# Performance work log

Measured on AMD Instinct MI355X. Metric: run time of the kernel, lower is better.

## Reference

```python
import jax, jax.numpy as jnp
import numpy as np

B, T, D = 2, 2048, 1024
H = 16
DH = D // H


def setup_inputs() -> dict:
    key = jax.random.key(0)
    ks = jax.random.split(key, 6)
    s = 1.0 / np.sqrt(D)
    return {
        "input_emb": jax.random.normal(ks[0], (B, T, D), dtype=jnp.float32),
        "W_key": jax.random.normal(ks[1], (D, D), dtype=jnp.float32) * s,
        "W_query": jax.random.normal(ks[2], (D, D), dtype=jnp.float32) * s,
        "W_value": jax.random.normal(ks[3], (D, D), dtype=jnp.float32) * s,
        "W_out": jax.random.normal(ks[4], (D, D), dtype=jnp.float32) * s,
        "b_out": jnp.zeros((D,), dtype=jnp.float32),
    }


def reference(input_emb, W_key, W_query, W_value, W_out, b_out):
    b, t, _ = input_emb.shape
    # projections (no bias on K/Q/V, matching bias_on=False)
    k = (input_emb @ W_key).reshape(b, t, H, DH).transpose(0, 2, 1, 3)    # [b,h,t,dh]
    q = (input_emb @ W_query).reshape(b, t, H, DH).transpose(0, 2, 1, 3)
    v = (input_emb @ W_value).reshape(b, t, H, DH).transpose(0, 2, 1, 3)
    # NOTE: source computes K @ Q^T (not Q @ K^T) — reproduce faithfully.
    scores = jnp.einsum("bhid,bhjd->bhij", k, q) / jnp.sqrt(jnp.float32(DH))
    mask = jnp.triu(jnp.ones((t, t), dtype=bool), k=1)                    # True where j > i
    scores = jnp.where(mask, -jnp.inf, scores)
    attn = jax.nn.softmax(scores, axis=-1)                                # softmax over j (query axis)
    ctx = jnp.einsum("bhij,bhjd->bhid", attn, v)                          # [b,h,t,dh]
    ctx = ctx.transpose(0, 2, 1, 3).reshape(b, t, H * DH)                 # [b,t,d]
    return ctx @ W_out + b_out
```

## Files before the change

kernel.cpp:

```cpp
#include <hip/hip_runtime.h>
#include <cstdint>
#include <cstddef>

#define T_SEQ 2048
#define DMODEL 1024
#define NHEAD 16
#define DHEAD 64
#define BATCH 2
#define MROWS (BATCH * T_SEQ)

typedef __attribute__((ext_vector_type(8))) short bf16x8;
typedef __attribute__((ext_vector_type(4))) float f32x4;
typedef unsigned int u32;

__device__ __forceinline__ unsigned short f2bf(float f) {
  u32 u = __float_as_uint(f);
  u32 r = (u + 0x7FFFu + ((u >> 16) & 1u)) >> 16;
  return (unsigned short)r;
}

__device__ __forceinline__ u32 cvtpk(float a, float b) {
  u32 r;
  asm("v_cvt_pk_bf16_f32 %0, %1, %2" : "=v"(r) : "v"(a), "v"(b));
  return r;
}

__device__ __forceinline__ void gl_lds16(const unsigned short* g, unsigned short* l) {
  __builtin_amdgcn_global_load_lds(
      (const __attribute__((address_space(1))) u32*)g,
      (__attribute__((address_space(3))) u32*)l, 16, 0, 0);
}

__global__ void k_cvt(const float* __restrict__ src, unsigned short* __restrict__ dst, int n) {
  int i = (blockIdx.x * 256 + threadIdx.x) * 4;
  if (i + 3 < n) {
    float4 v = *reinterpret_cast<const float4*>(src + i);
    ushort4 o;
    o.x = f2bf(v.x); o.y = f2bf(v.y); o.z = f2bf(v.z); o.w = f2bf(v.w);
    *reinterpret_cast<ushort4*>(dst + i) = o;
  }
}

__global__ void k_tc4(const float* __restrict__ W0, const float* __restrict__ W1,
                      const float* __restrict__ W2, const float* __restrict__ W3,
                      unsigned short* __restrict__ T0, unsigned short* __restrict__ T1,
                      unsigned short* __restrict__ T2, unsigned short* __restrict__ T3) {
  const int z = blockIdx.z;
  const float* W = (z == 0) ? W0 : (z == 1) ? W1 : (z == 2) ? W2 : W3;
  unsigned short* Wt = (z == 0) ? T0 : (z == 1) ? T1 : (z == 2) ? T2 : T3;
  __shared__ float tile[32][33];
  const int c0 = blockIdx.x * 32, r0 = blockIdx.y * 32;
  const int tx = threadIdx.x & 31, ty = threadIdx.x >> 5;
#pragma unroll
  for (int i = ty; i < 32; i += 8)
    tile[i][tx] = W[(size_t)(r0 + i) * DMODEL + c0 + tx];
  __syncthreads();
#pragma unroll
  for (int i = ty; i < 32; i += 8)
    Wt[(size_t)(c0 + i) * DMODEL + r0 + tx] = f2bf(tile[tx][i]);
}

__global__ __launch_bounds__(256, 2)
void k_gemm_qkv(const unsigned short* __restrict__ Xb,
                const unsigned short* __restrict__ Wkt,
                const unsigned short* __restrict__ Wqt,
                const unsigned short* __restrict__ Wvt,
                unsigned short* __restrict__ Qr,
                unsigned short* __restrict__ Kr,
                unsigned short* __restrict__ Vt)
{
  __shared__ __align__(16) unsigned short As[128 * 32];
  __shared__ __align__(16) unsigned short Bs[128 * 32];
  const int z = blockIdx.z;
  const unsigned short* Bt = (z == 0) ? Wkt : (z == 1) ? Wqt : Wvt;

  const int tid = threadIdx.x;
  const int lane = tid & 63, w = tid >> 6;
  const int wr = w >> 1, wc = w & 1;
  const int l15 = lane & 15, l4 = lane >> 4;
  const int m0 = blockIdx.y * 128, n0 = blockIdx.x * 128;

  f32x4 acc[4][4] = {};

  for (int k0 = 0; k0 < DMODEL; k0 += 32) {
#pragma unroll
    for (int i = 0; i < 2; ++i) {
      int c = i * 256 + tid;
      int row = c >> 2, cc = c & 3;
      gl_lds16(Xb + (size_t)(m0 + row) * DMODEL + k0 + cc * 8, As + c * 8);
      gl_lds16(Bt + (size_t)(n0 + row) * DMODEL + k0 + cc * 8, Bs + c * 8);
    }
    __syncthreads();
    bf16x8 af[4], bfr[4];
#pragma unroll
    for (int mi = 0; mi < 4; ++mi)
      af[mi] = *reinterpret_cast<const bf16x8*>(As + (wr * 64 + mi * 16 + l15) * 32 + l4 * 8);
#pragma unroll
    for (int ni = 0; ni < 4; ++ni)
      bfr[ni] = *reinterpret_cast<const bf16x8*>(Bs + (wc * 64 + ni * 16 + l15) * 32 + l4 * 8);
#pragma unroll
    for (int mi = 0; mi < 4; ++mi)
#pragma unroll
      for (int ni = 0; ni < 4; ++ni)
        acc[mi][ni] = __builtin_amdgcn_mfma_f32_16x16x32_bf16(af[mi], bfr[ni], acc[mi][ni], 0, 0, 0);
    __syncthreads();
  }

  if (z < 2) {
    unsigned short* C = (z == 0) ? Qr : Kr;
#pragma unroll
    for (int mi = 0; mi < 4; ++mi)
#pragma unroll
      for (int ni = 0; ni < 4; ++ni) {
        const int col = n0 + wc * 64 + ni * 16 + l15;
        const int rowb = m0 + wr * 64 + mi * 16 + l4 * 4;
#pragma unroll
        for (int r = 0; r < 4; ++r)
          C[(size_t)(rowb + r) * DMODEL + col] = f2bf(acc[mi][ni][r]);
      }
  } else {
#pragma unroll
    for (int mi = 0; mi < 4; ++mi)
#pragma unroll
      for (int ni = 0; ni < 4; ++ni) {
        const int col = n0 + wc * 64 + ni * 16 + l15;
        const int h = col >> 6, dh = col & 63;
        const int rowb = m0 + wr * 64 + mi * 16 + l4 * 4;
        const int b = rowb >> 11, t = rowb & (T_SEQ - 1);
        const int tl = t & 63;
        const int tp = (t & ~63) | (tl & 32) | ((tl & 12) << 1) | ((tl & 16) >> 2);
        unsigned short* p = Vt + ((size_t)(b * NHEAD + h) * DHEAD + dh) * T_SEQ + tp;
        ushort4 pkv;
        pkv.x = f2bf(acc[mi][ni][0]); pkv.y = f2bf(acc[mi][ni][1]);
        pkv.z = f2bf(acc[mi][ni][2]); pkv.w = f2bf(acc[mi][ni][3]);
        *reinterpret_cast<ushort4*>(p) = pkv;
      }
  }
}

__global__ __launch_bounds__(512, 2)
void k_attn(const unsigned short* __restrict__ Qr,
            const unsigned short* __restrict__ Kr,
            const unsigned short* __restrict__ Vp,
            unsigned short* __restrict__ ctx)
{
  __shared__ __align__(16) char lds[65536];
  const int tid = threadIdx.x;
  const int lane = tid & 63, w = tid >> 6;
  const int l15 = lane & 15, l4 = lane >> 4;

  const int x = blockIdx.x;
  const int xcd = x & 7, idx = x >> 3;
  const int bh = xcd + 8 * (idx & 3);
  const int cpair = idx >> 2;
  const int b = bh >> 4, h = bh & 15;

  const unsigned short* Qbase = Qr + (size_t)b * T_SEQ * DMODEL + h * DHEAD;
  const unsigned short* Kbase = Kr + (size_t)b * T_SEQ * DMODEL + h * DHEAD;
  const unsigned short* Vbase = Vp + (size_t)bh * DHEAD * T_SEQ;
  unsigned short* obase = ctx + (size_t)b * T_SEQ * DMODEL + h * DHEAD;

  const float SC = 0.18033688011112042f;
  const float M0 = 12.0f;
  const int srow = tid >> 3, scb = tid & 7;
  const int scolE = (scb ^ (srow & 7)) << 3;

  const int sw = (l15 & 7) << 4;
  const char* aK0 = lds + l15 * 128 + ((l4 * 16) ^ sw);
  const char* aK1 = lds + l15 * 128 + (((64 + l4 * 16)) ^ sw);

  const unsigned short* kp = Kbase + (size_t)srow * DMODEL + scolE;
  const unsigned short* vpb = Vbase + (size_t)srow * T_SEQ + scolE;

#define KRD(P, st, ni, v1) (*reinterpret_cast<const bf16x8*>(((v1) ? aK1 : aK0) + (P) * 16384 + (st) * 8192 + (ni) * 2048))
#define VRD(P, st, df, hk) (*reinterpret_cast<const bf16x8*>(((hk) ? aK1 : aK0) + 32768 + (P) * 16384 + (st) * 8192 + (df) * 2048))

#define GROUP_BODY(g, P)                                                          \
    {                                                                             \
      const int kv0 = (g) * 128;                                                  \
      const bool diag = ((g) == NG - 1);                                          \
      __builtin_amdgcn_sched_barrier(0);                                          \
      asm volatile("s_waitcnt vmcnt(0)" ::: "memory");                            \
      __builtin_amdgcn_sched_barrier(0);                                          \
      __builtin_amdgcn_s_barrier();                                               \
      __builtin_amdgcn_sched_barrier(0);                                          \
      if ((g) + 1 < NG) {                                                         \
        unsigned short* Kn = (unsigned short*)(lds + ((P) ^ 1) * 16384);          \
        unsigned short* Vn = (unsigned short*)(lds + 32768 + ((P) ^ 1) * 16384);  \
        gl_lds16(kstage, Kn + tid * 8);                                           \
        gl_lds16(kstage + 64 * DMODEL, Kn + 4096 + tid * 8);                      \
        gl_lds16(vstage, Vn + tid * 8);                                           \
        gl_lds16(vstage + 64, Vn + 4096 + tid * 8);                               \
        kstage += 128 * DMODEL; vstage += 128;                                    \
      }                                                                           \
      __builtin_amdgcn_sched_barrier(0);                                          \
      const bool a1 = !diag || (w >= 4);                                          \
      const int nlim0 = (diag && w < 4) ? (w + 1) : 4;                            \
      const int nlim1 = (diag && w >= 4) ? (w - 3) : 4;                           \
      f32x4 S[2][4] = {};                                                         \
      __builtin_amdgcn_s_setprio(1);                                              \
      _Pragma("unroll")                                                           \
      for (int ni = 0; ni < 4; ++ni)                                              \
        if (ni < nlim0) {                                                         \
          S[0][ni] = __builtin_amdgcn_mfma_f32_16x16x32_bf16(KRD(P, 0, ni, 0), qf[0], S[0][ni], 0, 0, 0); \
          S[0][ni] = __builtin_amdgcn_mfma_f32_16x16x32_bf16(KRD(P, 0, ni, 1), qf[1], S[0][ni], 0, 0, 0); \
        }                                                                         \
      if (a1) {                                                                   \
        _Pragma("unroll")                                                         \
        for (int ni = 0; ni < 4; ++ni)                                            \
          if (ni < nlim1) {                                                       \
            S[1][ni] = __builtin_amdgcn_mfma_f32_16x16x32_bf16(KRD(P, 1, ni, 0), qf[0], S[1][ni], 0, 0, 0); \
            S[1][ni] = __builtin_amdgcn_mfma_f32_16x16x32_bf16(KRD(P, 1, ni, 1), qf[1], S[1][ni], 0, 0, 0); \
          }                                                                       \
      }                                                                           \
      __builtin_amdgcn_s_setprio(0);                                              \
      if (diag) {                                                                 \
        const int st = (w < 4) ? 0 : 1;                                           \
        const int kvst = kv0 + st * 64;                                           \
        const int nl = (w < 4) ? nlim0 : nlim1;                                   \
        _Pragma("unroll")                                                         \
        for (int ni = 0; ni < 4; ++ni)                                            \
          if (ni < nl) {                                                          \
            _Pragma("unroll")                                                     \
            for (int r = 0; r < 4; ++r)                                           \
              if (kvst + ni * 16 + l4 * 4 + r > qrow) S[st][ni][r] = -INFINITY;   \
          }                                                                       \
      }                                                                           \
      union __align__(16) PW { u32 u[2][2][4]; bf16x8 v[2][2]; } pw = {};         \
      _Pragma("unroll")                                                           \
      for (int ni = 0; ni < 4; ++ni)                                              \
        if (ni < nlim0) {                                                         \
          const float p0 = __builtin_amdgcn_exp2f(__builtin_fmaf(S[0][ni][0], SC, -M0)); \
          const float p1 = __builtin_amdgcn_exp2f(__builtin_fmaf(S[0][ni][1], SC, -M0)); \
          const float p2 = __builtin_amdgcn_exp2f(__builtin_fmaf(S[0][ni][2], SC, -M0)); \
          const float p3 = __builtin_amdgcn_exp2f(__builtin_fmaf(S[0][ni][3], SC, -M0)); \
          lP += (p0 + p1) + (p2 + p3);                                            \
          pw.u[0][ni >> 1][(ni & 1) * 2]     = cvtpk(p0, p1);                     \
          pw.u[0][ni >> 1][(ni & 1) * 2 + 1] = cvtpk(p2, p3);                     \
        }                                                                         \
      if (a1) {                                                                   \
        _Pragma("unroll")                                                         \
        for (int ni = 0; ni < 4; ++ni)                                            \
          if (ni < nlim1) {                                                       \
            const float p0 = __builtin_amdgcn_exp2f(__builtin_fmaf(S[1][ni][0], SC, -M0)); \
            const float p1 = __builtin_amdgcn_exp2f(__builtin_fmaf(S[1][ni][1], SC, -M0)); \
            const float p2 = __builtin_amdgcn_exp2f(__builtin_fmaf(S[1][ni][2], SC, -M0)); \
            const float p3 = __builtin_amdgcn_exp2f(__builtin_fmaf(S[1][ni][3], SC, -M0)); \
            lP += (p0 + p1) + (p2 + p3);                                          \
            pw.u[1][ni >> 1][(ni & 1) * 2]     = cvtpk(p0, p1);                   \
            pw.u[1][ni >> 1][(ni & 1) * 2 + 1] = cvtpk(p2, p3);                   \
          }                                                                       \
      }                                                                           \
      __builtin_amdgcn_s_setprio(1);                                              \
      {                                                                           \
        const int hkl0 = (diag && w < 4) ? ((nlim0 + 1) >> 1) : 2;                \
        _Pragma("unroll")                                                         \
        for (int hk = 0; hk < 2; ++hk)                                            \
          if (hk < hkl0) {                                                        \
            _Pragma("unroll")                                                     \
            for (int df = 0; df < 4; ++df)                                        \
              O[df] = __builtin_amdgcn_mfma_f32_16x16x32_bf16(VRD(P, 0, df, hk), pw.v[0][hk], O[df], 0, 0, 0); \
          }                                                                       \
      }                                                                           \
      if (a1) {                                                                   \
        const int hkl1 = (diag && w >= 4) ? ((nlim1 + 1) >> 1) : 2;               \
        _Pragma("unroll")                                                         \
        for (int hk = 0; hk < 2; ++hk)                                            \
          if (hk < hkl1) {                                                        \
            _Pragma("unroll")                                                     \
            for (int df = 0; df < 4; ++df)                                        \
              O[df] = __builtin_amdgcn_mfma_f32_16x16x32_bf16(VRD(P, 1, df, hk), pw.v[1][hk], O[df], 0, 0, 0); \
          }                                                                       \
      }                                                                           \
      __builtin_amdgcn_s_setprio(0);                                              \
      __builtin_amdgcn_sched_barrier(0);                                          \
    }

  for (int half = 0; half < 2; ++half) {
    const int c = half ? (15 - cpair) : cpair;
    const int q0w = c * 128 + w * 16;
    const int NG = c + 1;
    const int qrow = q0w + l15;

    bf16x8 qf[2];
#pragma unroll
    for (int ks = 0; ks < 2; ++ks)
      qf[ks] = *reinterpret_cast<const bf16x8*>(
          Qbase + (size_t)(q0w + l15) * DMODEL + ks * 32 + l4 * 8);

    __builtin_amdgcn_sched_barrier(0);
    __builtin_amdgcn_s_barrier();
    __builtin_amdgcn_sched_barrier(0);
    {
      unsigned short* Ks = (unsigned short*)(lds);
      unsigned short* Vs = (unsigned short*)(lds + 32768);
      gl_lds16(kp, Ks + tid * 8);
      gl_lds16(kp + 64 * DMODEL, Ks + 4096 + tid * 8);
      gl_lds16(vpb, Vs + tid * 8);
      gl_lds16(vpb + 64, Vs + 4096 + tid * 8);
    }
    const unsigned short* kstage = kp + 128 * DMODEL;
    const unsigned short* vstage = vpb + 128;

    f32x4 O[4] = {};
    float lP = 0.f;

    for (int g2 = 0; g2 < NG; g2 += 2) {
      GROUP_BODY(g2, 0)
      if (g2 + 1 < NG) GROUP_BODY(g2 + 1, 1)
    }

    float lS = lP;
    lS += __shfl_xor(lS, 16);
    lS += __shfl_xor(lS, 32);
    const float rinv = 1.0f / lS;
#pragma unroll
    for (int df = 0; df < 4; ++df) {
      ushort4 o;
      o.x = f2bf(O[df][0] * rinv);
      o.y = f2bf(O[df][1] * rinv);
      o.z = f2bf(O[df][2] * rinv);
      o.w = f2bf(O[df][3] * rinv);
      *reinterpret_cast<ushort4*>(obase + (size_t)qrow * DMODEL + df * 16 + l4 * 4) = o;
    }
  }
#undef GROUP_BODY
#undef KRD
#undef VRD
}

__global__ __launch_bounds__(256, 2)
void k_gemm_out(const unsigned short* __restrict__ Ab,
                const unsigned short* __restrict__ Bt,
                const float* __restrict__ bias,
                float* __restrict__ C)
{
  __shared__ __align__(16) unsigned short As[128 * 32];
  __shared__ __align__(16) unsigned short Bs[128 * 32];
  const int tid = threadIdx.x;
  const int lane = tid & 63, w = tid >> 6;
  const int wr = w >> 1, wc = w & 1;
  const int l15 = lane & 15, l4 = lane >> 4;
  const int m0 = blockIdx.y * 128, n0 = blockIdx.x * 128;

  f32x4 acc[4][4] = {};

  for (int k0 = 0; k0 < DMODEL; k0 += 32) {
#pragma unroll
    for (int i = 0; i < 2; ++i) {
      int c = i * 256 + tid;
      int row = c >> 2, cc = c & 3;
      gl_lds16(Ab + (size_t)(m0 + row) * DMODEL + k0 + cc * 8, As + c * 8);
      gl_lds16(Bt + (size_t)(n0 + row) * DMODEL + k0 + cc * 8, Bs + c * 8);
    }
    __syncthreads();
    bf16x8 af[4], bfr[4];
#pragma unroll
    for (int mi = 0; mi < 4; ++mi)
      af[mi] = *reinterpret_cast<const bf16x8*>(As + (wr * 64 + mi * 16 + l15) * 32 + l4 * 8);
#pragma unroll
    for (int ni = 0; ni < 4; ++ni)
      bfr[ni] = *reinterpret_cast<const bf16x8*>(Bs + (wc * 64 + ni * 16 + l15) * 32 + l4 * 8);
#pragma unroll
    for (int mi = 0; mi < 4; ++mi)
#pragma unroll
      for (int ni = 0; ni < 4; ++ni)
        acc[mi][ni] = __builtin_amdgcn_mfma_f32_16x16x32_bf16(af[mi], bfr[ni], acc[mi][ni], 0, 0, 0);
    __syncthreads();
  }

#pragma unroll
  for (int mi = 0; mi < 4; ++mi)
#pragma unroll
    for (int ni = 0; ni < 4; ++ni) {
      const int col = n0 + wc * 64 + ni * 16 + l15;
      const float bv = bias[col];
      const int rowb = m0 + wr * 64 + mi * 16 + l4 * 4;
#pragma unroll
      for (int r = 0; r < 4; ++r)
        C[(size_t)(rowb + r) * DMODEL + col] = acc[mi][ni][r] + bv;
    }
}

extern "C" void kernel_launch(void* const* d_in, const int* in_sizes, int n_in,
                              void* d_out, int out_size, void* d_ws, size_t ws_size,
                              hipStream_t stream) {
  const float* X  = (const float*)d_in[0];
  const float* Wk = (const float*)d_in[1];
  const float* Wq = (const float*)d_in[2];
  const float* Wv = (const float*)d_in[3];
  const float* Wo = (const float*)d_in[4];
  const float* bo = (const float*)d_in[5];
  float* out = (float*)d_out;

  char* ws = (char*)d_ws;
  const size_t MB = 1024 * 1024;
  unsigned short* Xb  = (unsigned short*)(ws + 0 * MB);
  unsigned short* Wkt = (unsigned short*)(ws + 8 * MB);
  unsigned short* Wqt = (unsigned short*)(ws + 10 * MB);
  unsigned short* Wvt = (unsigned short*)(ws + 12 * MB);
  unsigned short* Wot = (unsigned short*)(ws + 14 * MB);
  unsigned short* Qr  = (unsigned short*)(ws + 16 * MB);
  unsigned short* Kr  = (unsigned short*)(ws + 24 * MB);
  unsigned short* Vt  = (unsigned short*)(ws + 32 * MB);
  unsigned short* Ctx = (unsigned short*)(ws + 40 * MB);

  k_cvt<<<4096, 256, 0, stream>>>(X, Xb, MROWS * DMODEL);
  k_tc4<<<dim3(32, 32, 4), 256, 0, stream>>>(Wk, Wq, Wv, Wo, Wkt, Wqt, Wvt, Wot);

  k_gemm_qkv<<<dim3(8, 32, 3), 256, 0, stream>>>(Xb, Wkt, Wqt, Wvt, Qr, Kr, Vt);
  k_attn<<<dim3(256), 512, 0, stream>>>(Qr, Kr, Vt, Ctx);
  k_gemm_out<<<dim3(8, 32), 256, 0, stream>>>(Ctx, Wot, bo, out);
}
```

Measured before the change: 107.3 us.

## Split attention waves over KV halves with two query tiles and LDS reduction

```diff
diff --git a/kernel.cpp b/kernel.cpp
--- a/kernel.cpp
+++ b/kernel.cpp
@@ -148,6 +148,7 @@
   const int tid = threadIdx.x;
   const int lane = tid & 63, w = tid >> 6;
   const int l15 = lane & 15, l4 = lane >> 4;
+  const int wsub = w & 3, par = w >> 2;
 
   const int x = blockIdx.x;
   const int xcd = x & 7, idx = x >> 3;
@@ -166,14 +167,15 @@
   const int scolE = (scb ^ (srow & 7)) << 3;
 
   const int sw = (l15 & 7) << 4;
-  const char* aK0 = lds + l15 * 128 + ((l4 * 16) ^ sw);
-  const char* aK1 = lds + l15 * 128 + (((64 + l4 * 16)) ^ sw);
+  const char* base0 = lds + par * 8192 + l15 * 128 + ((l4 * 16) ^ sw);
+  const char* base1 = lds + par * 8192 + l15 * 128 + ((64 + l4 * 16) ^ sw);
 
   const unsigned short* kp = Kbase + (size_t)srow * DMODEL + scolE;
   const unsigned short* vpb = Vbase + (size_t)srow * T_SEQ + scolE;
 
-#define KRD(P, st, ni, v1) (*reinterpret_cast<const bf16x8*>(((v1) ? aK1 : aK0) + (P) * 16384 + (st) * 8192 + (ni) * 2048))
-#define VRD(P, st, df, hk) (*reinterpret_cast<const bf16x8*>(((hk) ? aK1 : aK0) + 32768 + (P) * 16384 + (st) * 8192 + (df) * 2048))
+#define MFMA16(a, bq, c) __builtin_amdgcn_mfma_f32_16x16x32_bf16((a), (bq), (c), 0, 0, 0)
+#define KRD(P, ni, v1) (*reinterpret_cast<const bf16x8*>(((v1) ? base1 : base0) + (P) * 16384 + (ni) * 2048))
+#define VRD(P, df, hk) (*reinterpret_cast<const bf16x8*>(((hk) ? base1 : base0) + 32768 + (P) * 16384 + (df) * 2048))
 
 #define GROUP_BODY(g, P)                                                          \
     {                                                                             \
@@ -194,99 +196,97 @@
         kstage += 128 * DMODEL; vstage += 128;                                    \
       }                                                                           \
       __builtin_amdgcn_sched_barrier(0);                                          \
-      const bool a1 = !diag || (w >= 4);                                          \
-      const int nlim0 = (diag && w < 4) ? (w + 1) : 4;                            \
-      const int nlim1 = (diag && w >= 4) ? (w - 3) : 4;                           \
-      f32x4 S[2][4] = {};                                                         \
+      int nl0 = 4, nl1 = 4;                                                       \
+      if (diag) {                                                                 \
+        nl0 = ((wsub * 32 + 15 - par * 64) >> 4) + 1;                             \
+        nl1 = ((wsub * 32 + 31 - par * 64) >> 4) + 1;                             \
+        nl0 = nl0 < 0 ? 0 : (nl0 > 4 ? 4 : nl0);                                  \
+        nl1 = nl1 < 0 ? 0 : (nl1 > 4 ? 4 : nl1);                                  \
+      }                                                                           \
+      f32x4 S0[4] = {}, S1[4] = {};                                               \
       __builtin_amdgcn_s_setprio(1);                                              \
       _Pragma("unroll")                                                           \
       for (int ni = 0; ni < 4; ++ni)                                              \
-        if (ni < nlim0) {                                                         \
-          S[0][ni] = __builtin_amdgcn_mfma_f32_16x16x32_bf16(KRD(P, 0, ni, 0), qf[0], S[0][ni], 0, 0, 0); \
-          S[0][ni] = __builtin_amdgcn_mfma_f32_16x16x32_bf16(KRD(P, 0, ni, 1), qf[1], S[0][ni], 0, 0, 0); \
+        if (ni < nl1) {                                                           \
+          const bf16x8 ka = KRD(P, ni, 0);                                        \
+          const bf16x8 kb = KRD(P, ni, 1);                                        \
+          if (ni < nl0) {                                                         \
+            S0[ni] = MFMA16(ka, qf[0][0], S0[ni]);                                \
+            S0[ni] = MFMA16(kb, qf[0][1], S0[ni]);                                \
+          }                                                                       \
+          S1[ni] = MFMA16(ka, qf[1][0], S1[ni]);                                  \
+          S1[ni] = MFMA16(kb, qf[1][1], S1[ni]);                                  \
         }                                                                         \
-      if (a1) {                                                                   \
-        _Pragma("unroll")                                                         \
-        for (int ni = 0; ni < 4; ++ni)                                            \
-          if (ni < nlim1) {                                                       \
-            S[1][ni] = __builtin_amdgcn_mfma_f32_16x16x32_bf16(KRD(P, 1, ni, 0), qf[0], S[1][ni], 0, 0, 0); \
-            S[1][ni] = __builtin_amdgcn_mfma_f32_16x16x32_bf16(KRD(P, 1, ni, 1), qf[1], S[1][ni], 0, 0, 0); \
-          }                                                                       \
-      }                                                                           \
       __builtin_amdgcn_s_setprio(0);                                              \
       if (diag) {                                                                 \
-        const int st = (w < 4) ? 0 : 1;                                           \
-        const int kvst = kv0 + st * 64;                                           \
-        const int nl = (w < 4) ? nlim0 : nlim1;                                   \
+        const int kvb = kv0 + par * 64;                                           \
         _Pragma("unroll")                                                         \
-        for (int ni = 0; ni < 4; ++ni)                                            \
-          if (ni < nl) {                                                          \
-            _Pragma("unroll")                                                     \
-            for (int r = 0; r < 4; ++r)                                           \
-              if (kvst + ni * 16 + l4 * 4 + r > qrow) S[st][ni][r] = -INFINITY;   \
+        for (int ni = 0; ni < 4; ++ni) {                                          \
+          _Pragma("unroll")                                                       \
+          for (int r = 0; r < 4; ++r) {                                           \
+            const int kvi = kvb + ni * 16 + l4 * 4 + r;                           \
+            if (ni < nl0 && kvi > qrow0) S0[ni][r] = -INFINITY;                   \
+            if (ni < nl1 && kvi > qrow1) S1[ni][r] = -INFINITY;                   \
           }                                                                       \
+        }                                                                         \
       }                                                                           \
-      union __align__(16) PW { u32 u[2][2][4]; bf16x8 v[2][2]; } pw = {};         \
+      PW pw0 = {}, pw1 = {};                                                      \
       _Pragma("unroll")                                                           \
-      for (int ni = 0; ni < 4; ++ni)                                              \
-        if (ni < nlim0) {                                                         \
-          const float p0 = __builtin_amdgcn_exp2f(__builtin_fmaf(S[0][ni][0], SC, -M0)); \
-          const float p1 = __builtin_amdgcn_exp2f(__builtin_fmaf(S[0][ni][1], SC, -M0)); \
-          const float p2 = __builtin_amdgcn_exp2f(__builtin_fmaf(S[0][ni][2], SC, -M0)); \
-          const float p3 = __builtin_amdgcn_exp2f(__builtin_fmaf(S[0][ni][3], SC, -M0)); \
-          lP += (p0 + p1) + (p2 + p3);                                            \
-          pw.u[0][ni >> 1][(ni & 1) * 2]     = cvtpk(p0, p1);                     \
-          pw.u[0][ni >> 1][(ni & 1) * 2 + 1] = cvtpk(p2, p3);                     \
+      for (int ni = 0; ni < 4; ++ni) {                                            \
+        if (ni < nl0) {                                                           \
+          const float p0 = __builtin_amdgcn_exp2f(__builtin_fmaf(S0[ni][0], SC, -M0)); \
+          const float p1 = __builtin_amdgcn_exp2f(__builtin_fmaf(S0[ni][1], SC, -M0)); \
+          const float p2 = __builtin_amdgcn_exp2f(__builtin_fmaf(S0[ni][2], SC, -M0)); \
+          const float p3 = __builtin_amdgcn_exp2f(__builtin_fmaf(S0[ni][3], SC, -M0)); \
+          lP0 += (p0 + p1) + (p2 + p3);                                           \
+          pw0.u[ni >> 1][(ni & 1) * 2]     = cvtpk(p0, p1);                       \
+          pw0.u[ni >> 1][(ni & 1) * 2 + 1] = cvtpk(p2, p3);                       \
         }                                                                         \
-      if (a1) {                                                                   \
-        _Pragma("unroll")                                                         \
-        for (int ni = 0; ni < 4; ++ni)                                            \
-          if (ni < nlim1) {                                                       \
-            const float p0 = __builtin_amdgcn_exp2f(__builtin_fmaf(S[1][ni][0], SC, -M0)); \
-            const float p1 = __builtin_amdgcn_exp2f(__builtin_fmaf(S[1][ni][1], SC, -M0)); \
-            const float p2 = __builtin_amdgcn_exp2f(__builtin_fmaf(S[1][ni][2], SC, -M0)); \
-            const float p3 = __builtin_amdgcn_exp2f(__builtin_fmaf(S[1][ni][3], SC, -M0)); \
-            lP += (p0 + p1) + (p2 + p3);                                          \
-            pw.u[1][ni >> 1][(ni & 1) * 2]     = cvtpk(p0, p1);                   \
-            pw.u[1][ni >> 1][(ni & 1) * 2 + 1] = cvtpk(p2, p3);                   \
-          }                                                                       \
+        if (ni < nl1) {                                                           \
+          const float p0 = __builtin_amdgcn_exp2f(__builtin_fmaf(S1[ni][0], SC, -M0)); \
+          const float p1 = __builtin_amdgcn_exp2f(__builtin_fmaf(S1[ni][1], SC, -M0)); \
+          const float p2 = __builtin_amdgcn_exp2f(__builtin_fmaf(S1[ni][2], SC, -M0)); \
+          const float p3 = __builtin_amdgcn_exp2f(__builtin_fmaf(S1[ni][3], SC, -M0)); \
+          lP1 += (p0 + p1) + (p2 + p3);                                           \
+          pw1.u[ni >> 1][(ni & 1) * 2]     = cvtpk(p0, p1);                       \
+          pw1.u[ni >> 1][(ni & 1) * 2 + 1] = cvtpk(p2, p3);                       \
+        }                                                                         \
       }                                                                           \
       __builtin_amdgcn_s_setprio(1);                                              \
       {                                                                           \
-        const int hkl0 = (diag && w < 4) ? ((nlim0 + 1) >> 1) : 2;                \
-        _Pragma("unroll")                                                         \
-        for (int hk = 0; hk < 2; ++hk)                                            \
-          if (hk < hkl0) {                                                        \
-            _Pragma("unroll")                                                     \
-            for (int df = 0; df < 4; ++df)                                        \
-              O[df] = __builtin_amdgcn_mfma_f32_16x16x32_bf16(VRD(P, 0, df, hk), pw.v[0][hk], O[df], 0, 0, 0); \
-          }                                                                       \
-      }                                                                           \
-      if (a1) {                                                                   \
-        const int hkl1 = (diag && w >= 4) ? ((nlim1 + 1) >> 1) : 2;               \
+        const int hkl0 = diag ? ((nl0 + 1) >> 1) : 2;                             \
+        const int hkl1 = diag ? ((nl1 + 1) >> 1) : 2;                             \
         _Pragma("unroll")                                                         \
         for (int hk = 0; hk < 2; ++hk)                                            \
           if (hk < hkl1) {                                                        \
             _Pragma("unroll")                                                     \
-            for (int df = 0; df < 4; ++df)                                        \
-              O[df] = __builtin_amdgcn_mfma_f32_16x16x32_bf16(VRD(P, 1, df, hk), pw.v[1][hk], O[df], 0, 0, 0); \
+            for (int df = 0; df < 4; ++df) {                                      \
+              const bf16x8 vv = VRD(P, df, hk);                                   \
+              if (hk < hkl0) O0[df] = MFMA16(vv, pw0.v[hk], O0[df]);              \
+              O1[df] = MFMA16(vv, pw1.v[hk], O1[df]);                             \
+            }                                                                     \
           }                                                                       \
       }                                                                           \
       __builtin_amdgcn_s_setprio(0);                                              \
       __builtin_amdgcn_sched_barrier(0);                                          \
     }
 
+  union __align__(16) PW { u32 u[2][4]; bf16x8 v[2]; };
+
   for (int half = 0; half < 2; ++half) {
     const int c = half ? (15 - cpair) : cpair;
-    const int q0w = c * 128 + w * 16;
+    const int q0w = c * 128 + wsub * 32;
     const int NG = c + 1;
-    const int qrow = q0w + l15;
-
-    bf16x8 qf[2];
-#pragma unroll
-    for (int ks = 0; ks < 2; ++ks)
-      qf[ks] = *reinterpret_cast<const bf16x8*>(
-          Qbase + (size_t)(q0w + l15) * DMODEL + ks * 32 + l4 * 8);
+    const int qrow0 = q0w + l15;
+    const int qrow1 = q0w + 16 + l15;
+
+    bf16x8 qf[2][2];
+#pragma unroll
+    for (int qm = 0; qm < 2; ++qm)
+#pragma unroll
+      for (int ks = 0; ks < 2; ++ks)
+        qf[qm][ks] = *reinterpret_cast<const bf16x8*>(
+            Qbase + (size_t)(q0w + qm * 16 + l15) * DMODEL + ks * 32 + l4 * 8);
 
     __builtin_amdgcn_sched_barrier(0);
     __builtin_amdgcn_s_barrier();
@@ -302,31 +302,63 @@
     const unsigned short* kstage = kp + 128 * DMODEL;
     const unsigned short* vstage = vpb + 128;
 
-    f32x4 O[4] = {};
-    float lP = 0.f;
+    f32x4 O0[4] = {}, O1[4] = {};
+    float lP0 = 0.f, lP1 = 0.f;
 
     for (int g2 = 0; g2 < NG; g2 += 2) {
       GROUP_BODY(g2, 0)
       if (g2 + 1 < NG) GROUP_BODY(g2 + 1, 1)
     }
 
-    float lS = lP;
-    lS += __shfl_xor(lS, 16);
-    lS += __shfl_xor(lS, 32);
-    const float rinv = 1.0f / lS;
-#pragma unroll
-    for (int df = 0; df < 4; ++df) {
-      ushort4 o;
-      o.x = f2bf(O[df][0] * rinv);
-      o.y = f2bf(O[df][1] * rinv);
-      o.z = f2bf(O[df][2] * rinv);
-      o.w = f2bf(O[df][3] * rinv);
-      *reinterpret_cast<ushort4*>(obase + (size_t)qrow * DMODEL + df * 16 + l4 * 4) = o;
+    __builtin_amdgcn_sched_barrier(0);
+    __builtin_amdgcn_s_barrier();
+    float* scr = (float*)lds + ((size_t)(wsub * 64 + lane)) * 35;
+    if (par == 1) {
+#pragma unroll
+      for (int df = 0; df < 4; ++df)
+#pragma unroll
+        for (int r = 0; r < 4; ++r) {
+          scr[df * 4 + r] = O0[df][r];
+          scr[16 + df * 4 + r] = O1[df][r];
+        }
+      scr[32] = lP0; scr[33] = lP1;
+    }
+    __builtin_amdgcn_sched_barrier(0);
+    __builtin_amdgcn_s_barrier();
+    __builtin_amdgcn_sched_barrier(0);
+    if (par == 0) {
+#pragma unroll
+      for (int df = 0; df < 4; ++df)
+#pragma unroll
+        for (int r = 0; r < 4; ++r) {
+          O0[df][r] += scr[df * 4 + r];
+          O1[df][r] += scr[16 + df * 4 + r];
+        }
+      lP0 += scr[32]; lP1 += scr[33];
+      float lS0 = lP0;
+      lS0 += __shfl_xor(lS0, 16);
+      lS0 += __shfl_xor(lS0, 32);
+      float lS1 = lP1;
+      lS1 += __shfl_xor(lS1, 16);
+      lS1 += __shfl_xor(lS1, 32);
+      const float rinv0 = 1.0f / lS0;
+      const float rinv1 = 1.0f / lS1;
+#pragma unroll
+      for (int df = 0; df < 4; ++df) {
+        ushort4 o0, o1;
+        o0.x = f2bf(O0[df][0] * rinv0); o0.y = f2bf(O0[df][1] * rinv0);
+        o0.z = f2bf(O0[df][2] * rinv0); o0.w = f2bf(O0[df][3] * rinv0);
+        o1.x = f2bf(O1[df][0] * rinv1); o1.y = f2bf(O1[df][1] * rinv1);
+        o1.z = f2bf(O1[df][2] * rinv1); o1.w = f2bf(O1[df][3] * rinv1);
+        *reinterpret_cast<ushort4*>(obase + (size_t)qrow0 * DMODEL + df * 16 + l4 * 4) = o0;
+        *reinterpret_cast<ushort4*>(obase + (size_t)qrow1 * DMODEL + df * 16 + l4 * 4) = o1;
+      }
     }
   }
 #undef GROUP_BODY
 #undef KRD
 #undef VRD
+#undef MFMA16
 }
 
 __global__ __launch_bounds__(256, 2)
```

Measured after the change: 119.5 us. 1.11x slower.

## Merge prep kernels and remap GEMM block indices for XCD locality

Applied to the files above, without the earlier changes.

```diff
diff --git a/kernel.cpp b/kernel.cpp
--- a/kernel.cpp
+++ b/kernel.cpp
@@ -31,25 +31,28 @@
       (__attribute__((address_space(3))) u32*)l, 16, 0, 0);
 }
 
-__global__ void k_cvt(const float* __restrict__ src, unsigned short* __restrict__ dst, int n) {
-  int i = (blockIdx.x * 256 + threadIdx.x) * 4;
-  if (i + 3 < n) {
-    float4 v = *reinterpret_cast<const float4*>(src + i);
+__global__ void k_prep(const float* __restrict__ X, unsigned short* __restrict__ Xb,
+                       const float* __restrict__ W0, const float* __restrict__ W1,
+                       const float* __restrict__ W2, const float* __restrict__ W3,
+                       unsigned short* __restrict__ T0, unsigned short* __restrict__ T1,
+                       unsigned short* __restrict__ T2, unsigned short* __restrict__ T3) {
+  const int bid = blockIdx.x;
+  if (bid < 4096) {
+    int i = (bid * 256 + threadIdx.x) * 4;
+    float4 v = *reinterpret_cast<const float4*>(X + i);
     ushort4 o;
     o.x = f2bf(v.x); o.y = f2bf(v.y); o.z = f2bf(v.z); o.w = f2bf(v.w);
-    *reinterpret_cast<ushort4*>(dst + i) = o;
+    *reinterpret_cast<ushort4*>(Xb + i) = o;
+    return;
   }
-}
-
-__global__ void k_tc4(const float* __restrict__ W0, const float* __restrict__ W1,
-                      const float* __restrict__ W2, const float* __restrict__ W3,
-                      unsigned short* __restrict__ T0, unsigned short* __restrict__ T1,
-                      unsigned short* __restrict__ T2, unsigned short* __restrict__ T3) {
-  const int z = blockIdx.z;
+  const int b2 = bid - 4096;
+  const int z = b2 >> 10;
+  const int rem = b2 & 1023;
+  const int cx = rem & 31, ry = rem >> 5;
   const float* W = (z == 0) ? W0 : (z == 1) ? W1 : (z == 2) ? W2 : W3;
   unsigned short* Wt = (z == 0) ? T0 : (z == 1) ? T1 : (z == 2) ? T2 : T3;
   __shared__ float tile[32][33];
-  const int c0 = blockIdx.x * 32, r0 = blockIdx.y * 32;
+  const int c0 = cx * 32, r0 = ry * 32;
   const int tx = threadIdx.x & 31, ty = threadIdx.x >> 5;
 #pragma unroll
   for (int i = ty; i < 32; i += 8)
@@ -71,14 +74,18 @@
 {
   __shared__ __align__(16) unsigned short As[128 * 32];
   __shared__ __align__(16) unsigned short Bs[128 * 32];
-  const int z = blockIdx.z;
+  const int orig = blockIdx.x;
+  const int t = (orig & 7) * 96 + (orig >> 3);
+  const int z = t >> 8;
+  const int remt = t & 255;
+  const int by = remt >> 3, bx = remt & 7;
   const unsigned short* Bt = (z == 0) ? Wkt : (z == 1) ? Wqt : Wvt;
 
   const int tid = threadIdx.x;
   const int lane = tid & 63, w = tid >> 6;
   const int wr = w >> 1, wc = w & 1;
   const int l15 = lane & 15, l4 = lane >> 4;
-  const int m0 = blockIdx.y * 128, n0 = blockIdx.x * 128;
+  const int m0 = by * 128, n0 = bx * 128;
 
   f32x4 acc[4][4] = {};
 
@@ -126,9 +133,9 @@
         const int col = n0 + wc * 64 + ni * 16 + l15;
         const int h = col >> 6, dh = col & 63;
         const int rowb = m0 + wr * 64 + mi * 16 + l4 * 4;
-        const int b = rowb >> 11, t = rowb & (T_SEQ - 1);
-        const int tl = t & 63;
-        const int tp = (t & ~63) | (tl & 32) | ((tl & 12) << 1) | ((tl & 16) >> 2);
+        const int b = rowb >> 11, tt = rowb & (T_SEQ - 1);
+        const int tl = tt & 63;
+        const int tp = (tt & ~63) | (tl & 32) | ((tl & 12) << 1) | ((tl & 16) >> 2);
         unsigned short* p = Vt + ((size_t)(b * NHEAD + h) * DHEAD + dh) * T_SEQ + tp;
         ushort4 pkv;
         pkv.x = f2bf(acc[mi][ni][0]); pkv.y = f2bf(acc[mi][ni][1]);
@@ -337,11 +344,15 @@
 {
   __shared__ __align__(16) unsigned short As[128 * 32];
   __shared__ __align__(16) unsigned short Bs[128 * 32];
+  const int orig = blockIdx.x;
+  const int t = (orig & 7) * 32 + (orig >> 3);
+  const int by = t >> 3, bx = t & 7;
+
   const int tid = threadIdx.x;
   const int lane = tid & 63, w = tid >> 6;
   const int wr = w >> 1, wc = w & 1;
   const int l15 = lane & 15, l4 = lane >> 4;
-  const int m0 = blockIdx.y * 128, n0 = blockIdx.x * 128;
+  const int m0 = by * 128, n0 = bx * 128;
 
   f32x4 acc[4][4] = {};
 
@@ -405,10 +416,8 @@
   unsigned short* Vt  = (unsigned short*)(ws + 32 * MB);
   unsigned short* Ctx = (unsigned short*)(ws + 40 * MB);
 
-  k_cvt<<<4096, 256, 0, stream>>>(X, Xb, MROWS * DMODEL);
-  k_tc4<<<dim3(32, 32, 4), 256, 0, stream>>>(Wk, Wq, Wv, Wo, Wkt, Wqt, Wvt, Wot);
-
-  k_gemm_qkv<<<dim3(8, 32, 3), 256, 0, stream>>>(Xb, Wkt, Wqt, Wvt, Qr, Kr, Vt);
+  k_prep<<<8192, 256, 0, stream>>>(X, Xb, Wk, Wq, Wv, Wo, Wkt, Wqt, Wvt, Wot);
+  k_gemm_qkv<<<768, 256, 0, stream>>>(Xb, Wkt, Wqt, Wvt, Qr, Kr, Vt);
   k_attn<<<dim3(256), 512, 0, stream>>>(Qr, Kr, Vt, Ctx);
-  k_gemm_out<<<dim3(8, 32), 256, 0, stream>>>(Ctx, Wot, bo, out);
-}
+  k_gemm_out<<<256, 256, 0, stream>>>(Ctx, Wot, bo, out);
+}
```

Result: faster. 104.9 us (-2.2%).
